# Kernel optimization log

Measured on AMD Instinct MI355X. Metric: run time of the kernel, lower is better.

The kernel has to match this reference:

```python
import jax, jax.numpy as jnp
import numpy as np

N, D, M = 65536, 1024, 32768

def setup_inputs() -> dict:
    key = jax.random.key(0)
    k1, k2, k3, k4, k5 = jax.random.split(key, 5)
    var = jax.random.randint(k1, (N, D), -128, 128, dtype=jnp.int8)
    var_scale = jax.random.uniform(k2, (1,), jnp.float32) * 0.02 + 0.01
    indices = jax.random.randint(k3, (M, D), 0, N, dtype=jnp.int32)
    updates = (jax.random.normal(k4, (M, D)) ).astype(jnp.float16)
    smooth_scales = (jax.random.uniform(k5, (D,)) + 0.5).astype(jnp.float16)
    return {"var": var, "var_scale": var_scale, "indices": indices,
            "updates": updates, "smooth_scales": smooth_scales}

def reference(var, var_scale, indices, updates, smooth_scales):
    # dequantize int8 var with fp32 scale
    out = var.astype(jnp.float32) * var_scale  # [N, D]
    # smooth-scale the updates, promote to fp32
    upd = (updates * smooth_scales).astype(jnp.float32)  # [M, D]
    # torch scatter_add_ along axis 0: out[indices[i,j], j] += upd[i,j]
    cols = jnp.arange(out.shape[1])[None, :]  # [1, D] broadcasts vs [M, D] indices
    out = out.at[indices, cols].add(upd)
    # global abs-max -> dynamic requantization to int8
    max_val = jnp.max(jnp.abs(out))
    new_scale = max_val / 127.0
    y = jnp.clip(jnp.round(out / new_scale), -128, 127).astype(jnp.int8)
    return (y, out, new_scale[None])
```

## Files before the change

### kernel.cpp

```cpp
#include <hip/hip_runtime.h>
#include <hip/hip_fp16.h>

#define N_ROWS 65536
#define D_COLS 1024
#define M_ROWS 32768
#define QROWS  16384

using u32 = unsigned int;
using u16 = unsigned short;
typedef float f32x4 __attribute__((ext_vector_type(4)));
typedef int   i32x4 __attribute__((ext_vector_type(4)));

__global__ void init_ws_k(u32* ws) {
    if (threadIdx.x == 0 && blockIdx.x == 0) ws[0] = 0u;
}

__global__ __launch_bounds__(256) void t_idx_upd_k(const int* __restrict__ idx,
                                                   const float* __restrict__ upd,
                                                   const float* __restrict__ scl,
                                                   u16* __restrict__ idxT,
                                                   __half* __restrict__ updT) {
    __shared__ u32   sidx[64][65];
    __shared__ float supd[64][65];
    const int swz = (int)(blockIdx.x & 7) * 1024 + (int)(blockIdx.x >> 3);
    const int i0 = (swz & 511) * 64;
    const int j0 = (swz >> 9) * 64;
    const int t = threadIdx.x;

    {
        const int rr = t >> 2, c4 = t & 3;
        const int*   ip = idx + (size_t)(i0 + rr) * D_COLS + j0;
        const float* up = upd + (size_t)(i0 + rr) * D_COLS + j0;
        #pragma unroll
        for (int cq = 0; cq < 4; ++cq) {
            const int jc = cq * 16 + c4 * 4;
            const i32x4 iv = __builtin_nontemporal_load((const i32x4*)(ip + jc));
            const f32x4 uv = __builtin_nontemporal_load((const f32x4*)(up + jc));
            sidx[rr][jc] = (u32)iv.x; sidx[rr][jc+1] = (u32)iv.y;
            sidx[rr][jc+2] = (u32)iv.z; sidx[rr][jc+3] = (u32)iv.w;
            supd[rr][jc] = uv.x; supd[rr][jc+1] = uv.y;
            supd[rr][jc+2] = uv.z; supd[rr][jc+3] = uv.w;
        }
    }
    __syncthreads();

    {
        const int jj = t >> 2, seg = t & 3;
        const __half hs = __float2half(scl[j0 + jj]);
        u32 wi[8], wh[8];
        #pragma unroll
        for (int p = 0; p < 8; ++p) {
            const int r = seg * 16 + 2 * p;
            const u32 a = sidx[r][jj] & 0xffffu, b = sidx[r + 1][jj] & 0xffffu;
            wi[p] = a | (b << 16);
            const __half2 h2 = __halves2half2(__hmul(__float2half(supd[r][jj]), hs),
                                              __hmul(__float2half(supd[r + 1][jj]), hs));
            wh[p] = *reinterpret_cast<const u32*>(&h2);
        }
        u16* di = idxT + (size_t)(j0 + jj) * M_ROWS + i0 + seg * 16;
        __half* dh = updT + (size_t)(j0 + jj) * M_ROWS + i0 + seg * 16;
        ((uint4*)di)[0] = uint4{wi[0], wi[1], wi[2], wi[3]};
        ((uint4*)di)[1] = uint4{wi[4], wi[5], wi[6], wi[7]};
        ((uint4*)dh)[0] = uint4{wh[0], wh[1], wh[2], wh[3]};
        ((uint4*)dh)[1] = uint4{wh[4], wh[5], wh[6], wh[7]};
    }
}

__global__ __launch_bounds__(1024) void scatter_q_k(const u16* __restrict__ idxT,
                                                    const __half* __restrict__ updT,
                                                    __half* __restrict__ sumT) {
    __shared__ float acc[QROWS];
    const int bid = (blockIdx.x & 7) * 512 + (blockIdx.x >> 3);
    const int j = bid >> 2;
    const int h = bid & 3;
    const int tid = threadIdx.x;

    float4* acc4 = (float4*)acc;
    for (int t = tid; t < QROWS / 4; t += 1024) acc4[t] = float4{0.f, 0.f, 0.f, 0.f};

    const int4* ip4 = (const int4*)(idxT + (size_t)j * M_ROWS);
    const int4* up4 = (const int4*)(updT + (size_t)j * M_ROWS);
    __syncthreads();

    #pragma unroll
    for (int k = 0; k < 4; ++k) {
        const int t = k * 1024 + tid;
        const int4 iv = ip4[t];
        const int4 uv = up4[t];
        const u32 iw[4] = {(u32)iv.x, (u32)iv.y, (u32)iv.z, (u32)iv.w};
        const u32 uw[4] = {(u32)uv.x, (u32)uv.y, (u32)uv.z, (u32)uv.w};
        #pragma unroll
        for (int e = 0; e < 4; ++e) {
            const int r0 = iw[e] & 0xffff, r1 = iw[e] >> 16;
            const __half2 h2 = *reinterpret_cast<const __half2*>(&uw[e]);
            if ((r0 >> 14) == h)
                unsafeAtomicAdd(&acc[r0 & (QROWS - 1)], __half2float(__low2half(h2)));
            if ((r1 >> 14) == h)
                unsafeAtomicAdd(&acc[r1 & (QROWS - 1)], __half2float(__high2half(h2)));
        }
    }
    __syncthreads();

    __half2* dst = (__half2*)(sumT + (size_t)j * N_ROWS + h * QROWS);
    for (int t = tid; t < QROWS / 2; t += 1024)
        dst[t] = __floats2half2_rn(acc[2 * t], acc[2 * t + 1]);
}

__global__ __launch_bounds__(256) void finalize_k(const int* __restrict__ var,
                                                  const __half* __restrict__ sumT,
                                                  const float* __restrict__ var_scale,
                                                  float* __restrict__ outf,
                                                  u32* __restrict__ ws) {
    __shared__ float sm[64][68];
    __shared__ float wmax[4];
    const int swz = (int)(blockIdx.x & 7) * 2048 + (int)(blockIdx.x >> 3);
    const int r0 = (swz & 1023) * 64;
    const int j0 = (swz >> 10) * 64;
    const int tid = threadIdx.x;
    const float s = var_scale[0];

    {
        const int jj = tid >> 2, seg = tid & 3;
        const __half* colp = sumT + (size_t)(j0 + jj) * N_ROWS + r0 + seg * 16;
        #pragma unroll
        for (int q = 0; q < 2; ++q) {
            const uint4 w = ((const uint4*)colp)[q];
            const u32 wv[4] = {w.x, w.y, w.z, w.w};
            #pragma unroll
            for (int i = 0; i < 4; ++i) {
                const __half2 hh = *reinterpret_cast<const __half2*>(&wv[i]);
                const float2 f = __half22float2(hh);
                const int rr = seg * 16 + q * 8 + i * 2;
                sm[rr][jj] = f.x;
                sm[rr + 1][jj] = f.y;
            }
        }
    }
    __syncthreads();

    float m = 0.f;
    #pragma unroll
    for (int k = 0; k < 4; ++k) {
        const int l = k * 256 + tid;
        const int rr = l >> 4, c4 = l & 15;
        const i32x4 v = __builtin_nontemporal_load(
            (const i32x4*)(var + (size_t)(r0 + rr) * D_COLS + j0) + c4);
        const float4 sv = *(const float4*)&sm[rr][c4 * 4];
        float4 o;
        o.x = (float)v.x * s + sv.x;
        o.y = (float)v.y * s + sv.y;
        o.z = (float)v.z * s + sv.z;
        o.w = (float)v.w * s + sv.w;
        ((float4*)(outf + (size_t)(r0 + rr) * D_COLS + j0))[c4] = o;
        m = fmaxf(m, fmaxf(fmaxf(fabsf(o.x), fabsf(o.y)),
                           fmaxf(fabsf(o.z), fabsf(o.w))));
    }
    for (int off = 32; off; off >>= 1) m = fmaxf(m, __shfl_xor(m, off));
    if ((tid & 63) == 0) wmax[tid >> 6] = m;
    __syncthreads();
    if (tid == 0) {
        m = fmaxf(fmaxf(wmax[0], wmax[1]), fmaxf(wmax[2], wmax[3]));
        atomicMax(ws, __float_as_uint(m));
    }
}

__global__ __launch_bounds__(256) void quant_k(const float* __restrict__ outf,
                                               float* __restrict__ y,
                                               const u32* __restrict__ ws,
                                               float* __restrict__ scale_out) {
    const float mx = __uint_as_float(ws[0]);
    const float inv = 127.0f / mx;
    const int swz = (int)(blockIdx.x & 7) * 2048 + (int)(blockIdx.x >> 3);
    const int r0 = (swz & 1023) * 64;
    const int j0 = (swz >> 10) * 64;
    const int tid = threadIdx.x;
    if (blockIdx.x == 0 && tid == 0) scale_out[0] = mx / 127.0f;
    #pragma unroll
    for (int k = 0; k < 4; ++k) {
        const int l = k * 256 + tid;
        const int rr = l >> 4, c4 = l & 15;
        const size_t off = (size_t)(r0 + rr) * D_COLS + j0 + c4 * 4;
        const float4 v = *(const float4*)(outf + off);
        f32x4 o;
        o.x = fminf(fmaxf(rintf(v.x * inv), -128.f), 127.f);
        o.y = fminf(fmaxf(rintf(v.y * inv), -128.f), 127.f);
        o.z = fminf(fmaxf(rintf(v.z * inv), -128.f), 127.f);
        o.w = fminf(fmaxf(rintf(v.w * inv), -128.f), 127.f);
        __builtin_nontemporal_store(o, (f32x4*)(y + off));
    }
}

extern "C" void kernel_launch(void* const* d_in, const int* in_sizes, int n_in,
                              void* d_out, int out_size, void* d_ws, size_t ws_size,
                              hipStream_t stream) {
    const int*   var       = (const int*)d_in[0];
    const float* var_scale = (const float*)d_in[1];
    const int*   idx       = (const int*)d_in[2];
    const float* upd       = (const float*)d_in[3];
    const float* scl       = (const float*)d_in[4];

    float* y    = (float*)d_out;
    float* outf = y + (size_t)N_ROWS * D_COLS;
    float* scale_out = y + 2 * (size_t)N_ROWS * D_COLS;

    char* scratch = (char*)y;
    u16*    idxT = (u16*)scratch;
    __half* updT = (__half*)(scratch + (size_t)67108864);
    __half* sumT = (__half*)(scratch + (size_t)134217728);
    u32* ws = (u32*)d_ws;

    init_ws_k<<<1, 64, 0, stream>>>(ws);
    t_idx_upd_k<<<8192, 256, 0, stream>>>(idx, upd, scl, idxT, updT);
    scatter_q_k<<<4096, 1024, 0, stream>>>(idxT, updT, sumT);
    finalize_k<<<16384, 256, 0, stream>>>(var, sumT, var_scale, outf, ws);
    quant_k<<<16384, 256, 0, stream>>>(outf, y, ws, scale_out);
}
```

Baseline: 576.8 us.

## Pack index/update pairs and scatter into half-column LDS accumulators

The transpose kernel now emits a single 32-bit word per element holding the 16-bit row index and the fp16 scaled update, replacing the two separate streams. The scatter kernel splits each column into two halves of 32768 rows, using 128KB of LDS per block instead of four quarters. Each column's packed data is therefore read twice instead of four times, and the block count drops from 4096 to 2048. In exchange, the larger LDS footprint limits occupancy to about one block per CU, and every element now does an atomic add (zero for out-of-half rows) instead of a branch.

```diff
diff --git a/kernel.cpp b/kernel.cpp
--- a/kernel.cpp
+++ b/kernel.cpp
@@ -4,7 +4,7 @@
 #define N_ROWS 65536
 #define D_COLS 1024
 #define M_ROWS 32768
-#define QROWS  16384
+#define HROWS  32768
 
 using u32 = unsigned int;
 using u16 = unsigned short;
@@ -15,11 +15,10 @@
     if (threadIdx.x == 0 && blockIdx.x == 0) ws[0] = 0u;
 }
 
-__global__ __launch_bounds__(256) void t_idx_upd_k(const int* __restrict__ idx,
-                                                   const float* __restrict__ upd,
-                                                   const float* __restrict__ scl,
-                                                   u16* __restrict__ idxT,
-                                                   __half* __restrict__ updT) {
+__global__ __launch_bounds__(256) void t_pack_k(const int* __restrict__ idx,
+                                                const float* __restrict__ upd,
+                                                const float* __restrict__ scl,
+                                                u32* __restrict__ packed) {
     __shared__ u32   sidx[64][65];
     __shared__ float supd[64][65];
     const int swz = (int)(blockIdx.x & 7) * 1024 + (int)(blockIdx.x >> 3);
@@ -47,63 +46,65 @@
     {
         const int jj = t >> 2, seg = t & 3;
         const __half hs = __float2half(scl[j0 + jj]);
-        u32 wi[8], wh[8];
-        #pragma unroll
-        for (int p = 0; p < 8; ++p) {
-            const int r = seg * 16 + 2 * p;
-            const u32 a = sidx[r][jj] & 0xffffu, b = sidx[r + 1][jj] & 0xffffu;
-            wi[p] = a | (b << 16);
-            const __half2 h2 = __halves2half2(__hmul(__float2half(supd[r][jj]), hs),
-                                              __hmul(__float2half(supd[r + 1][jj]), hs));
-            wh[p] = *reinterpret_cast<const u32*>(&h2);
-        }
-        u16* di = idxT + (size_t)(j0 + jj) * M_ROWS + i0 + seg * 16;
-        __half* dh = updT + (size_t)(j0 + jj) * M_ROWS + i0 + seg * 16;
-        ((uint4*)di)[0] = uint4{wi[0], wi[1], wi[2], wi[3]};
-        ((uint4*)di)[1] = uint4{wi[4], wi[5], wi[6], wi[7]};
-        ((uint4*)dh)[0] = uint4{wh[0], wh[1], wh[2], wh[3]};
-        ((uint4*)dh)[1] = uint4{wh[4], wh[5], wh[6], wh[7]};
-    }
-}
-
-__global__ __launch_bounds__(1024) void scatter_q_k(const u16* __restrict__ idxT,
-                                                    const __half* __restrict__ updT,
+        u32 w16[16];
+        #pragma unroll
+        for (int p = 0; p < 16; ++p) {
+            const int r = seg * 16 + p;
+            const __half hv = __hmul(__float2half(supd[r][jj]), hs);
+            w16[p] = (sidx[r][jj] & 0xffffu) | ((u32)__half_as_ushort(hv) << 16);
+        }
+        u32* d = packed + (size_t)(j0 + jj) * M_ROWS + i0 + seg * 16;
+        ((uint4*)d)[0] = uint4{w16[0],  w16[1],  w16[2],  w16[3]};
+        ((uint4*)d)[1] = uint4{w16[4],  w16[5],  w16[6],  w16[7]};
+        ((uint4*)d)[2] = uint4{w16[8],  w16[9],  w16[10], w16[11]};
+        ((uint4*)d)[3] = uint4{w16[12], w16[13], w16[14], w16[15]};
+    }
+}
+
+__global__ __launch_bounds__(1024) void scatter_h_k(const u32* __restrict__ packed,
                                                     __half* __restrict__ sumT) {
-    __shared__ float acc[QROWS];
-    const int bid = (blockIdx.x & 7) * 512 + (blockIdx.x >> 3);
-    const int j = bid >> 2;
-    const int h = bid & 3;
+    __shared__ float acc[HROWS];
+    const int bid = (int)(blockIdx.x & 7) * 256 + (int)(blockIdx.x >> 3);
+    const int j = bid >> 1;
+    const int h = bid & 1;
     const int tid = threadIdx.x;
 
-    float4* acc4 = (float4*)acc;
-    for (int t = tid; t < QROWS / 4; t += 1024) acc4[t] = float4{0.f, 0.f, 0.f, 0.f};
-
-    const int4* ip4 = (const int4*)(idxT + (size_t)j * M_ROWS);
-    const int4* up4 = (const int4*)(updT + (size_t)j * M_ROWS);
-    __syncthreads();
-
-    #pragma unroll
-    for (int k = 0; k < 4; ++k) {
-        const int t = k * 1024 + tid;
-        const int4 iv = ip4[t];
-        const int4 uv = up4[t];
-        const u32 iw[4] = {(u32)iv.x, (u32)iv.y, (u32)iv.z, (u32)iv.w};
-        const u32 uw[4] = {(u32)uv.x, (u32)uv.y, (u32)uv.z, (u32)uv.w};
-        #pragma unroll
-        for (int e = 0; e < 4; ++e) {
-            const int r0 = iw[e] & 0xffff, r1 = iw[e] >> 16;
-            const __half2 h2 = *reinterpret_cast<const __half2*>(&uw[e]);
-            if ((r0 >> 14) == h)
-                unsafeAtomicAdd(&acc[r0 & (QROWS - 1)], __half2float(__low2half(h2)));
-            if ((r1 >> 14) == h)
-                unsafeAtomicAdd(&acc[r1 & (QROWS - 1)], __half2float(__high2half(h2)));
-        }
-    }
-    __syncthreads();
-
-    __half2* dst = (__half2*)(sumT + (size_t)j * N_ROWS + h * QROWS);
-    for (int t = tid; t < QROWS / 2; t += 1024)
-        dst[t] = __floats2half2_rn(acc[2 * t], acc[2 * t + 1]);
+    float4* a4 = (float4*)acc;
+    #pragma unroll
+    for (int k = 0; k < 8; ++k) a4[k * 1024 + tid] = float4{0.f, 0.f, 0.f, 0.f};
+
+    const i32x4* col4 = (const i32x4*)(packed + (size_t)j * M_ROWS);
+    i32x4 v[8];
+    #pragma unroll
+    for (int k = 0; k < 8; ++k) v[k] = col4[k * 1024 + tid];
+    __syncthreads();
+
+    #pragma unroll
+    for (int k = 0; k < 8; ++k) {
+        const u32 e[4] = {(u32)v[k].x, (u32)v[k].y, (u32)v[k].z, (u32)v[k].w};
+        #pragma unroll
+        for (int q = 0; q < 4; ++q) {
+            const int r = (int)(e[q] & 0xffffu);
+            float val = __half2float(__ushort_as_half((u16)(e[q] >> 16)));
+            val = ((r >> 15) == h) ? val : 0.0f;
+            atomicAdd(&acc[r & (HROWS - 1)], val);
+        }
+    }
+    __syncthreads();
+
+    uint4* dst4 = (uint4*)(sumT + (size_t)j * N_ROWS + h * HROWS);
+    #pragma unroll
+    for (int o = 0; o < 4; ++o) {
+        const int base = o * 8192 + tid * 8;
+        const float4 f0 = *(const float4*)&acc[base];
+        const float4 f1 = *(const float4*)&acc[base + 4];
+        const __half2 h0 = __floats2half2_rn(f0.x, f0.y);
+        const __half2 h1 = __floats2half2_rn(f0.z, f0.w);
+        const __half2 h2 = __floats2half2_rn(f1.x, f1.y);
+        const __half2 h3 = __floats2half2_rn(f1.z, f1.w);
+        dst4[o * 1024 + tid] = uint4{*(const u32*)&h0, *(const u32*)&h1,
+                                     *(const u32*)&h2, *(const u32*)&h3};
+    }
 }
 
 __global__ __launch_bounds__(256) void finalize_k(const int* __restrict__ var,
@@ -203,15 +204,13 @@
     float* outf = y + (size_t)N_ROWS * D_COLS;
     float* scale_out = y + 2 * (size_t)N_ROWS * D_COLS;
 
-    char* scratch = (char*)y;
-    u16*    idxT = (u16*)scratch;
-    __half* updT = (__half*)(scratch + (size_t)67108864);
-    __half* sumT = (__half*)(scratch + (size_t)134217728);
+    u32*    packed = (u32*)y;
+    __half* sumT   = (__half*)((char*)y + (size_t)134217728);
     u32* ws = (u32*)d_ws;
 
     init_ws_k<<<1, 64, 0, stream>>>(ws);
-    t_idx_upd_k<<<8192, 256, 0, stream>>>(idx, upd, scl, idxT, updT);
-    scatter_q_k<<<4096, 1024, 0, stream>>>(idxT, updT, sumT);
+    t_pack_k<<<8192, 256, 0, stream>>>(idx, upd, scl, packed);
+    scatter_h_k<<<2048, 1024, 0, stream>>>(packed, sumT);
     finalize_k<<<16384, 256, 0, stream>>>(var, sumT, var_scale, outf, ws);
     quant_k<<<16384, 256, 0, stream>>>(outf, y, ws, scale_out);
 }
```

After: 754.7 us. +30.9%, slower.
